# Kernel optimization log

Hardware: AMD Instinct MI355X
Metric: run time of the kernel (lower is better)

Reference implementation:

```python
import jax, jax.numpy as jnp
import numpy as np

N, E, D, L, R, G, C = 50000, 800000, 64, 3, 2, 128, 10


def setup_inputs() -> dict:
    key = jax.random.key(0)
    ks = jax.random.split(key, 16)
    s = 0.05
    x = jax.random.normal(ks[0], (N, D), dtype=jnp.float32)
    edge_index = jax.random.randint(ks[1], (2, E), 0, N, dtype=jnp.int64)
    edge_type = jax.random.randint(ks[2], (E,), 0, R, dtype=jnp.int64)
    batch = jnp.sort(jax.random.randint(ks[3], (N,), 0, G, dtype=jnp.int64))
    # per-layer self-loop Linear, per-(layer,relation) GIN eps + 2-layer MLP
    self_W = jax.random.normal(ks[4], (L, D, D), dtype=jnp.float32) * s
    self_b = jax.random.normal(ks[5], (L, D), dtype=jnp.float32) * s
    eps = jnp.zeros((L, R), dtype=jnp.float32)  # eps=0, train_eps=True
    mlp_W1 = jax.random.normal(ks[6], (L, R, D, D), dtype=jnp.float32) * s
    mlp_b1 = jax.random.normal(ks[7], (L, R, D), dtype=jnp.float32) * s
    mlp_W2 = jax.random.normal(ks[8], (L, R, D, D), dtype=jnp.float32) * s
    mlp_b2 = jax.random.normal(ks[9], (L, R, D), dtype=jnp.float32) * s
    lin1_W = jax.random.normal(ks[10], (D, D), dtype=jnp.float32) * s
    lin1_b = jax.random.normal(ks[11], (D,), dtype=jnp.float32) * s
    lin2_W = jax.random.normal(ks[12], (D, C), dtype=jnp.float32) * s
    lin2_b = jax.random.normal(ks[13], (C,), dtype=jnp.float32) * s
    return {"x": x, "edge_index": edge_index, "edge_type": edge_type, "batch": batch,
            "self_W": self_W, "self_b": self_b, "eps": eps,
            "mlp_W1": mlp_W1, "mlp_b1": mlp_b1, "mlp_W2": mlp_W2, "mlp_b2": mlp_b2,
            "lin1_W": lin1_W, "lin1_b": lin1_b, "lin2_W": lin2_W, "lin2_b": lin2_b}


def reference(x, edge_index, edge_type, batch, self_W, self_b, eps,
              mlp_W1, mlp_b1, mlp_W2, mlp_b2, lin1_W, lin1_b, lin2_W, lin2_b):
    src, dst = edge_index[0], edge_index[1]
    h = x
    for l in range(L):
        x_new = h @ self_W[l] + self_b[l]
        x_src = h[src]  # [E, D] gather of source features, done once per layer
        for r in range(R):
            # per-relation edge masking + scatter-add aggregation
            msg = jnp.where((edge_type == r)[:, None], x_src, jnp.zeros((), h.dtype))
            agg = jax.ops.segment_sum(msg, dst, num_segments=N)  # [N, D]
            z = (1.0 + eps[l, r]) * h + agg  # GIN combine
            z = jax.nn.relu(z @ mlp_W1[l, r] + mlp_b1[l, r])
            x_new = x_new + (z @ mlp_W2[l, r] + mlp_b2[l, r])
        h = x_new
    # global mean pooling over graphs
    sums = jax.ops.segment_sum(h, batch, num_segments=G)  # [G, D]
    counts = jax.ops.segment_sum(jnp.ones((N,), h.dtype), batch, num_segments=G)
    pooled = sums / jnp.maximum(counts, 1.0)[:, None]
    out = jax.nn.relu(pooled @ lin1_W + lin1_b)
    # dropout omitted (eval mode)
    out = out @ lin2_W + lin2_b
    return out
```

## Files before the change

### kernel.cpp

```cpp
#include <hip/hip_runtime.h>

#define Nn 50000
#define Dd 64
#define Ee 800000
#define Ll 3
#define Rr 2
#define Gg 128
#define Cc 10
#define NR (Nn * Rr)
#define NB ((NR + 1023) / 1024)
#define NT (Nn / 16)

typedef __attribute__((ext_vector_type(8))) short short8;
typedef __attribute__((ext_vector_type(4))) float f32x4;

__device__ __forceinline__ unsigned short bf16_rne(float x) {
  unsigned u = __float_as_uint(x);
  unsigned r = u + 0x7fffu + ((u >> 16) & 1u);
  return (unsigned short)(r >> 16);
}
__device__ __forceinline__ float bf16_tof(unsigned short b) {
  return __uint_as_float(((unsigned)b) << 16);
}

__global__ __launch_bounds__(256) void k_hist(
    const int* __restrict__ dst, const int* __restrict__ et,
    int* __restrict__ counts)
{
  int e = blockIdx.x * 256 + threadIdx.x;
  if (e >= Ee) return;
  atomicAdd(&counts[et[e] * Nn + dst[e]], 1);
}

__global__ __launch_bounds__(1024) void k_scan1(
    const int* __restrict__ counts, int* __restrict__ offs,
    int* __restrict__ btot)
{
  __shared__ int s[1024];
  int i = blockIdx.x * 1024 + threadIdx.x;
  int v = (i < NR) ? counts[i] : 0;
  s[threadIdx.x] = v;
  __syncthreads();
#pragma unroll
  for (int d = 1; d < 1024; d <<= 1) {
    int t = (threadIdx.x >= d) ? s[threadIdx.x - d] : 0;
    __syncthreads();
    s[threadIdx.x] += t;
    __syncthreads();
  }
  if (i < NR) offs[i + 1] = s[threadIdx.x];
  if (threadIdx.x == 1023) btot[blockIdx.x] = s[1023];
}

__global__ __launch_bounds__(128) void k_scan2(
    const int* __restrict__ btot, int* __restrict__ bscan)
{
  __shared__ int s[128];
  int v = (threadIdx.x < NB) ? btot[threadIdx.x] : 0;
  s[threadIdx.x] = v;
  __syncthreads();
#pragma unroll
  for (int d = 1; d < 128; d <<= 1) {
    int t = (threadIdx.x >= d) ? s[threadIdx.x - d] : 0;
    __syncthreads();
    s[threadIdx.x] += t;
    __syncthreads();
  }
  if (threadIdx.x < NB) bscan[threadIdx.x] = s[threadIdx.x] - v;
}

__global__ __launch_bounds__(1024) void k_scan3(
    const int* __restrict__ counts, const int* __restrict__ bscan,
    int* __restrict__ offs, int* __restrict__ cursor)
{
  int i = blockIdx.x * 1024 + threadIdx.x;
  if (i >= NR) return;
  int o = offs[i + 1] + bscan[blockIdx.x];
  offs[i + 1] = o;
  cursor[i] = o - counts[i];
  if (i == 0) offs[0] = 0;
}

__global__ __launch_bounds__(256) void k_fill(
    const int* __restrict__ src, const int* __restrict__ dst,
    const int* __restrict__ et, int* __restrict__ cursor,
    int* __restrict__ elist)
{
  int e = blockIdx.x * 256 + threadIdx.x;
  if (e >= Ee) return;
  int pos = atomicAdd(&cursor[et[e] * Nn + dst[e]], 1);
  elist[pos] = src[e];
}

__global__ __launch_bounds__(256) void k_prep(
    const float* __restrict__ selfW, const float* __restrict__ W1,
    const float* __restrict__ W2, unsigned short* __restrict__ wtHi,
    unsigned short* __restrict__ wtLo)
{
  int i = blockIdx.x * 256 + threadIdx.x;
  if (i >= Ll * 5 * 4096) return;
  int l = i / (5 * 4096);
  int rem = i - l * 5 * 4096;
  int m = rem >> 12;
  int e = rem & 4095;
  int k = e >> 6, c = e & 63;
  const float* p;
  if (m == 0)      p = selfW + (size_t)l * 4096;
  else if (m == 1) p = W1 + ((size_t)l * 2 + 0) * 4096;
  else if (m == 2) p = W2 + ((size_t)l * 2 + 0) * 4096;
  else if (m == 3) p = W1 + ((size_t)l * 2 + 1) * 4096;
  else             p = W2 + ((size_t)l * 2 + 1) * 4096;
  float w = p[e];
  unsigned short hi = bf16_rne(w);
  unsigned short lo = bf16_rne(w - bf16_tof(hi));
  size_t o = ((size_t)(l * 5 + m) * 64 + c) * 64 + k;
  wtHi[o] = hi;
  wtLo[o] = lo;
}

#define WOFF(m, c, ks) ((size_t)(m)*4096 + (size_t)(c)*64 + (ks)*32 + koff)

__global__ __launch_bounds__(128, 6) void k_update(
    const float* __restrict__ h, const int* __restrict__ offs,
    const int* __restrict__ elist,
    const unsigned short* __restrict__ wtHi, const unsigned short* __restrict__ wtLo,
    const float* __restrict__ selfb, const float* __restrict__ eps,
    const float* __restrict__ b1, const float* __restrict__ b2,
    float* __restrict__ hn, int l)
{
  __shared__ __align__(16) unsigned short tbh[2][16 * 72];
  __shared__ __align__(16) unsigned short tbl[2][16 * 72];
  __shared__ float xfer[16 * 65];
  const int wave = threadIdx.x >> 6;
  const int lane = threadIdx.x & 63;
  const int task = blockIdx.x;
  const int r = wave;
  const int idx15 = lane & 15;
  const int kg = lane >> 4;
  const int koff = kg * 8;
  const int nodeA = task * 16 + idx15;

  float f[2][8];
  {
    const float* hp = &h[(size_t)nodeA * 64 + koff];
    const float4 a0 = *(const float4*)(hp);
    const float4 a1 = *(const float4*)(hp + 4);
    const float4 b0 = *(const float4*)(hp + 32);
    const float4 b1v = *(const float4*)(hp + 36);
    f[0][0] = a0.x; f[0][1] = a0.y; f[0][2] = a0.z; f[0][3] = a0.w;
    f[0][4] = a1.x; f[0][5] = a1.y; f[0][6] = a1.z; f[0][7] = a1.w;
    f[1][0] = b0.x; f[1][1] = b0.y; f[1][2] = b0.z; f[1][3] = b0.w;
    f[1][4] = b1v.x; f[1][5] = b1v.y; f[1][6] = b1v.z; f[1][7] = b1v.w;
  }

  const unsigned short* whi = wtHi + (size_t)l * 5 * 4096;
  const unsigned short* wlo = wtLo + (size_t)l * 5 * 4096;
  const int m1 = 1 + 2 * r, m2 = 2 + 2 * r;
  const float er = 1.0f + eps[l * Rr + r];

  float za[2][8];
#pragma unroll
  for (int ks = 0; ks < 2; ++ks)
#pragma unroll
    for (int j = 0; j < 8; ++j) za[ks][j] = 0.0f;
  {
    int aidx = r * Nn + nodeA;
    int jb = offs[aidx], je = offs[aidx + 1];
    int j = jb;
    for (; j + 3 < je; j += 4) {
      int s0 = elist[j], s1 = elist[j + 1], s2 = elist[j + 2], s3 = elist[j + 3];
      const float* p0 = &h[(size_t)s0 * 64 + koff];
      const float* p1 = &h[(size_t)s1 * 64 + koff];
      const float* p2 = &h[(size_t)s2 * 64 + koff];
      const float* p3 = &h[(size_t)s3 * 64 + koff];
      const float4 a0 = *(const float4*)(p0),     a1 = *(const float4*)(p1);
      const float4 a2 = *(const float4*)(p2),     a3 = *(const float4*)(p3);
      const float4 b0 = *(const float4*)(p0 + 4), b1q = *(const float4*)(p1 + 4);
      const float4 b2q = *(const float4*)(p2 + 4), b3 = *(const float4*)(p3 + 4);
      const float4 c0 = *(const float4*)(p0 + 32), c1 = *(const float4*)(p1 + 32);
      const float4 c2 = *(const float4*)(p2 + 32), c3 = *(const float4*)(p3 + 32);
      const float4 d0 = *(const float4*)(p0 + 36), d1 = *(const float4*)(p1 + 36);
      const float4 d2 = *(const float4*)(p2 + 36), d3 = *(const float4*)(p3 + 36);
      za[0][0] += (a0.x + a1.x) + (a2.x + a3.x);
      za[0][1] += (a0.y + a1.y) + (a2.y + a3.y);
      za[0][2] += (a0.z + a1.z) + (a2.z + a3.z);
      za[0][3] += (a0.w + a1.w) + (a2.w + a3.w);
      za[0][4] += (b0.x + b1q.x) + (b2q.x + b3.x);
      za[0][5] += (b0.y + b1q.y) + (b2q.y + b3.y);
      za[0][6] += (b0.z + b1q.z) + (b2q.z + b3.z);
      za[0][7] += (b0.w + b1q.w) + (b2q.w + b3.w);
      za[1][0] += (c0.x + c1.x) + (c2.x + c3.x);
      za[1][1] += (c0.y + c1.y) + (c2.y + c3.y);
      za[1][2] += (c0.z + c1.z) + (c2.z + c3.z);
      za[1][3] += (c0.w + c1.w) + (c2.w + c3.w);
      za[1][4] += (d0.x + d1.x) + (d2.x + d3.x);
      za[1][5] += (d0.y + d1.y) + (d2.y + d3.y);
      za[1][6] += (d0.z + d1.z) + (d2.z + d3.z);
      za[1][7] += (d0.w + d1.w) + (d2.w + d3.w);
    }
    for (; j < je; ++j) {
      int sn = elist[j];
      const float* hp = &h[(size_t)sn * 64 + koff];
      const float4 a0 = *(const float4*)(hp);
      const float4 a1 = *(const float4*)(hp + 4);
      const float4 b0 = *(const float4*)(hp + 32);
      const float4 b1v = *(const float4*)(hp + 36);
      za[0][0] += a0.x; za[0][1] += a0.y; za[0][2] += a0.z; za[0][3] += a0.w;
      za[0][4] += a1.x; za[0][5] += a1.y; za[0][6] += a1.z; za[0][7] += a1.w;
      za[1][0] += b0.x; za[1][1] += b0.y; za[1][2] += b0.z; za[1][3] += b0.w;
      za[1][4] += b1v.x; za[1][5] += b1v.y; za[1][6] += b1v.z; za[1][7] += b1v.w;
    }
  }

  short8 zhi[2], zlo[2];
#pragma unroll
  for (int ks = 0; ks < 2; ++ks)
#pragma unroll
    for (int j = 0; j < 8; ++j) {
      float zf = er * f[ks][j] + za[ks][j];
      unsigned short hb = bf16_rne(zf);
      zhi[ks][j] = (short)hb;
      zlo[ks][j] = (short)bf16_rne(zf - bf16_tof(hb));
    }

  f32x4 tacc[4];
#pragma unroll
  for (int cb = 0; cb < 4; ++cb) {
    float bi = b1[((size_t)l * 2 + r) * 64 + cb * 16 + idx15];
    tacc[cb] = (f32x4){bi, bi, bi, bi};
  }
#pragma unroll
  for (int cb = 0; cb < 4; ++cb) {
    int c = cb * 16 + idx15;
#pragma unroll
    for (int ks = 0; ks < 2; ++ks) {
      const short8 bh = *(const short8*)&whi[WOFF(m1, c, ks)];
      const short8 bl = *(const short8*)&wlo[WOFF(m1, c, ks)];
      tacc[cb] = __builtin_amdgcn_mfma_f32_16x16x32_bf16(zhi[ks], bh, tacc[cb], 0, 0, 0);
      tacc[cb] = __builtin_amdgcn_mfma_f32_16x16x32_bf16(zhi[ks], bl, tacc[cb], 0, 0, 0);
      tacc[cb] = __builtin_amdgcn_mfma_f32_16x16x32_bf16(zlo[ks], bh, tacc[cb], 0, 0, 0);
    }
  }
#pragma unroll
  for (int cb = 0; cb < 4; ++cb)
#pragma unroll
    for (int q = 0; q < 4; ++q) {
      float tv = fmaxf(tacc[cb][q], 0.0f);
      unsigned short hb = bf16_rne(tv);
      tbh[wave][(kg * 4 + q) * 72 + cb * 16 + idx15] = hb;
      tbl[wave][(kg * 4 + q) * 72 + cb * 16 + idx15] = bf16_rne(tv - bf16_tof(hb));
    }
  asm volatile("s_waitcnt lgkmcnt(0)" ::: "memory");
  __builtin_amdgcn_sched_barrier(0);
  short8 thi[2], tlo[2];
#pragma unroll
  for (int ks = 0; ks < 2; ++ks) {
    thi[ks] = *(const short8*)&tbh[wave][idx15 * 72 + ks * 32 + koff];
    tlo[ks] = *(const short8*)&tbl[wave][idx15 * 72 + ks * 32 + koff];
  }

  f32x4 facc[4];
#pragma unroll
  for (int cb = 0; cb < 4; ++cb) {
    int c = cb * 16 + idx15;
    float bi = b2[((size_t)l * 2 + r) * 64 + c];
    if (wave == 1) bi += selfb[l * 64 + c];
    facc[cb] = (f32x4){bi, bi, bi, bi};
  }
#pragma unroll
  for (int cb = 0; cb < 4; ++cb) {
    int c = cb * 16 + idx15;
#pragma unroll
    for (int ks = 0; ks < 2; ++ks) {
      const short8 bh = *(const short8*)&whi[WOFF(m2, c, ks)];
      const short8 bl = *(const short8*)&wlo[WOFF(m2, c, ks)];
      facc[cb] = __builtin_amdgcn_mfma_f32_16x16x32_bf16(thi[ks], bh, facc[cb], 0, 0, 0);
      facc[cb] = __builtin_amdgcn_mfma_f32_16x16x32_bf16(thi[ks], bl, facc[cb], 0, 0, 0);
      facc[cb] = __builtin_amdgcn_mfma_f32_16x16x32_bf16(tlo[ks], bh, facc[cb], 0, 0, 0);
    }
  }
  if (wave == 1) {
    short8 ahi[2], alo[2];
#pragma unroll
    for (int ks = 0; ks < 2; ++ks)
#pragma unroll
      for (int j = 0; j < 8; ++j) {
        unsigned short hb = bf16_rne(f[ks][j]);
        ahi[ks][j] = (short)hb;
        alo[ks][j] = (short)bf16_rne(f[ks][j] - bf16_tof(hb));
      }
#pragma unroll
    for (int cb = 0; cb < 4; ++cb) {
      int c = cb * 16 + idx15;
#pragma unroll
      for (int ks = 0; ks < 2; ++ks) {
        const short8 bh = *(const short8*)&whi[WOFF(0, c, ks)];
        const short8 bl = *(const short8*)&wlo[WOFF(0, c, ks)];
        facc[cb] = __builtin_amdgcn_mfma_f32_16x16x32_bf16(ahi[ks], bh, facc[cb], 0, 0, 0);
        facc[cb] = __builtin_amdgcn_mfma_f32_16x16x32_bf16(ahi[ks], bl, facc[cb], 0, 0, 0);
        facc[cb] = __builtin_amdgcn_mfma_f32_16x16x32_bf16(alo[ks], bh, facc[cb], 0, 0, 0);
      }
    }
#pragma unroll
    for (int cb = 0; cb < 4; ++cb)
#pragma unroll
      for (int q = 0; q < 4; ++q)
        xfer[(kg * 4 + q) * 65 + cb * 16 + idx15] = facc[cb][q];
  }
  __syncthreads();
  if (wave == 0) {
#pragma unroll
    for (int cb = 0; cb < 4; ++cb)
#pragma unroll
      for (int q = 0; q < 4; ++q) {
        int row = kg * 4 + q, col = cb * 16 + idx15;
        hn[((size_t)task * 16 + row) * 64 + col] =
            facc[cb][q] + xfer[row * 65 + col];
      }
  }
}

__global__ __launch_bounds__(256) void k_pool(
    const float* __restrict__ h, const int* __restrict__ batch,
    float* __restrict__ sums, float* __restrict__ cnts)
{
  int w = blockIdx.x * 4 + (threadIdx.x >> 6);
  int lane = threadIdx.x & 63;
  int start = w * 64;
  if (start >= Nn) return;
  int cnt = min(64, Nn - start);
  int bg = batch[min(start + lane, Nn - 1)];
  int cur = __shfl(bg, 0, 64);
  float acc = 0.0f;
  int run = 0;
  for (int i = 0; i < cnt; ++i) {
    int g = __shfl(bg, i, 64);
    float v = h[(size_t)(start + i) * 64 + lane];
    if (g != cur) {
      atomicAdd(&sums[(size_t)cur * 64 + lane], acc);
      if (lane == 0) atomicAdd(&cnts[cur], (float)run);
      acc = 0.0f; run = 0; cur = g;
    }
    acc += v; run++;
  }
  atomicAdd(&sums[(size_t)cur * 64 + lane], acc);
  if (lane == 0) atomicAdd(&cnts[cur], (float)run);
}

__global__ __launch_bounds__(256) void k_head(
    const float* __restrict__ sums, const float* __restrict__ cnts,
    const float* __restrict__ l1W, const float* __restrict__ l1b,
    const float* __restrict__ l2W, const float* __restrict__ l2b,
    float* __restrict__ out)
{
  int wave = threadIdx.x >> 6;
  int lane = threadIdx.x & 63;
  int g = blockIdx.x * 4 + wave;
  if (g >= Gg) return;
  float p = sums[(size_t)g * Dd + lane] / fmaxf(cnts[g], 1.0f);
  float t = l1b[lane];
#pragma unroll
  for (int k = 0; k < Dd; ++k)
    t += __shfl(p, k, 64) * l1W[k * Dd + lane];
  t = fmaxf(t, 0.0f);
  float o = (lane < Cc) ? l2b[lane] : 0.0f;
#pragma unroll
  for (int k = 0; k < Dd; ++k) {
    float w = (lane < Cc) ? l2W[k * Cc + lane] : 0.0f;
    o += __shfl(t, k, 64) * w;
  }
  if (lane < Cc) out[(size_t)g * Cc + lane] = o;
}

extern "C" void kernel_launch(void* const* d_in, const int* in_sizes, int n_in,
                              void* d_out, int out_size, void* d_ws, size_t ws_size,
                              hipStream_t stream)
{
  const float* x     = (const float*)d_in[0];
  const int*   ei    = (const int*)d_in[1];
  const int*   et    = (const int*)d_in[2];
  const int*   batch = (const int*)d_in[3];
  const float* selfW = (const float*)d_in[4];
  const float* selfb = (const float*)d_in[5];
  const float* eps   = (const float*)d_in[6];
  const float* W1    = (const float*)d_in[7];
  const float* b1    = (const float*)d_in[8];
  const float* W2    = (const float*)d_in[9];
  const float* b2    = (const float*)d_in[10];
  const float* l1W   = (const float*)d_in[11];
  const float* l1b   = (const float*)d_in[12];
  const float* l2W   = (const float*)d_in[13];
  const float* l2b   = (const float*)d_in[14];
  float* out = (float*)d_out;

  float* buf0 = (float*)d_ws;
  float* buf1 = buf0 + (size_t)Nn * Dd;
  float* sums = buf1 + (size_t)Nn * Dd;
  float* cnts = sums + (size_t)Gg * Dd;
  unsigned short* wtHi = (unsigned short*)(cnts + Gg);
  unsigned short* wtLo = wtHi + (size_t)Ll * 5 * 4096;
  int* counts = (int*)(wtLo + (size_t)Ll * 5 * 4096);
  int* offs   = counts + NR;
  int* cursor = offs + NR + 1;
  int* btot   = cursor + NR;
  int* bscan  = btot + NB;
  int* elist  = bscan + NB;

  const int* src = ei;
  const int* dst = ei + Ee;

  hipMemsetAsync(sums, 0, (size_t)(Gg * Dd + Gg) * sizeof(float), stream);
  hipMemsetAsync(counts, 0, (size_t)NR * sizeof(int), stream);
  k_prep<<<(Ll * 5 * 4096 + 255) / 256, 256, 0, stream>>>(selfW, W1, W2, wtHi, wtLo);

  k_hist<<<(Ee + 255) / 256, 256, 0, stream>>>(dst, et, counts);
  k_scan1<<<NB, 1024, 0, stream>>>(counts, offs, btot);
  k_scan2<<<1, 128, 0, stream>>>(btot, bscan);
  k_scan3<<<NB, 1024, 0, stream>>>(counts, bscan, offs, cursor);
  k_fill<<<(Ee + 255) / 256, 256, 0, stream>>>(src, dst, et, cursor, elist);

  const float* h = x;
  float* hn = buf0;
  for (int l = 0; l < Ll; ++l) {
    k_update<<<NT, 128, 0, stream>>>(h, offs, elist, wtHi, wtLo,
                                     selfb, eps, b1, b2, hn, l);
    h = hn;
    hn = (hn == buf0) ? buf1 : buf0;
  }
  k_pool<<<(Nn / 64 + 4) / 4, 256, 0, stream>>>(h, batch, sums, cnts);
  k_head<<<32, 256, 0, stream>>>(sums, cnts, l1W, l1b, l2W, l2b, out);
}
```

Baseline: 338.1 us.

## Gather neighbor features from a bf16 shadow copy to halve gather bandwidth

Keeps a bf16 copy of node features alongside the fp32 buffer. Each layer writes both, and a new conversion kernel fills it for the input. The edge aggregation gathers bf16 rows, which halves the bytes read per neighbor in the bandwidth-bound gather. In exchange it adds an extra store per layer and a conversion pass, lowers the occupancy hint from 6 to 5, and loses precision in the aggregated sums, since neighbors are summed at bf16 resolution.

```diff
diff --git a/kernel.cpp b/kernel.cpp
--- a/kernel.cpp
+++ b/kernel.cpp
@@ -22,6 +22,16 @@
 __device__ __forceinline__ float bf16_tof(unsigned short b) {
   return __uint_as_float(((unsigned)b) << 16);
 }
+__device__ __forceinline__ void acc8(float* z, uint4 u) {
+  z[0] += __uint_as_float(u.x << 16);
+  z[1] += __uint_as_float(u.x & 0xffff0000u);
+  z[2] += __uint_as_float(u.y << 16);
+  z[3] += __uint_as_float(u.y & 0xffff0000u);
+  z[4] += __uint_as_float(u.z << 16);
+  z[5] += __uint_as_float(u.z & 0xffff0000u);
+  z[6] += __uint_as_float(u.w << 16);
+  z[7] += __uint_as_float(u.w & 0xffff0000u);
+}
 
 __global__ __launch_bounds__(256) void k_hist(
     const int* __restrict__ dst, const int* __restrict__ et,
@@ -90,6 +100,18 @@
   if (e >= Ee) return;
   int pos = atomicAdd(&cursor[et[e] * Nn + dst[e]], 1);
   elist[pos] = src[e];
+}
+
+__global__ __launch_bounds__(256) void k_cvt(
+    const float* __restrict__ x, unsigned short* __restrict__ hb)
+{
+  int i = blockIdx.x * 256 + threadIdx.x;
+  if (i >= (Nn * Dd) / 4) return;
+  const float4 v = *(const float4*)&x[(size_t)i * 4];
+  ushort4 o;
+  o.x = bf16_rne(v.x); o.y = bf16_rne(v.y);
+  o.z = bf16_rne(v.z); o.w = bf16_rne(v.w);
+  *(ushort4*)&hb[(size_t)i * 4] = o;
 }
 
 __global__ __launch_bounds__(256) void k_prep(
@@ -120,13 +142,13 @@
 
 #define WOFF(m, c, ks) ((size_t)(m)*4096 + (size_t)(c)*64 + (ks)*32 + koff)
 
-__global__ __launch_bounds__(128, 6) void k_update(
-    const float* __restrict__ h, const int* __restrict__ offs,
-    const int* __restrict__ elist,
+__global__ __launch_bounds__(128, 5) void k_update(
+    const float* __restrict__ h, const unsigned short* __restrict__ hb,
+    const int* __restrict__ offs, const int* __restrict__ elist,
     const unsigned short* __restrict__ wtHi, const unsigned short* __restrict__ wtLo,
     const float* __restrict__ selfb, const float* __restrict__ eps,
     const float* __restrict__ b1, const float* __restrict__ b2,
-    float* __restrict__ hn, int l)
+    float* __restrict__ hn, unsigned short* __restrict__ hnb, int l)
 {
   __shared__ __align__(16) unsigned short tbh[2][16 * 72];
   __shared__ __align__(16) unsigned short tbl[2][16 * 72];
@@ -169,46 +191,26 @@
     int j = jb;
     for (; j + 3 < je; j += 4) {
       int s0 = elist[j], s1 = elist[j + 1], s2 = elist[j + 2], s3 = elist[j + 3];
-      const float* p0 = &h[(size_t)s0 * 64 + koff];
-      const float* p1 = &h[(size_t)s1 * 64 + koff];
-      const float* p2 = &h[(size_t)s2 * 64 + koff];
-      const float* p3 = &h[(size_t)s3 * 64 + koff];
-      const float4 a0 = *(const float4*)(p0),     a1 = *(const float4*)(p1);
-      const float4 a2 = *(const float4*)(p2),     a3 = *(const float4*)(p3);
-      const float4 b0 = *(const float4*)(p0 + 4), b1q = *(const float4*)(p1 + 4);
-      const float4 b2q = *(const float4*)(p2 + 4), b3 = *(const float4*)(p3 + 4);
-      const float4 c0 = *(const float4*)(p0 + 32), c1 = *(const float4*)(p1 + 32);
-      const float4 c2 = *(const float4*)(p2 + 32), c3 = *(const float4*)(p3 + 32);
-      const float4 d0 = *(const float4*)(p0 + 36), d1 = *(const float4*)(p1 + 36);
-      const float4 d2 = *(const float4*)(p2 + 36), d3 = *(const float4*)(p3 + 36);
-      za[0][0] += (a0.x + a1.x) + (a2.x + a3.x);
-      za[0][1] += (a0.y + a1.y) + (a2.y + a3.y);
-      za[0][2] += (a0.z + a1.z) + (a2.z + a3.z);
-      za[0][3] += (a0.w + a1.w) + (a2.w + a3.w);
-      za[0][4] += (b0.x + b1q.x) + (b2q.x + b3.x);
-      za[0][5] += (b0.y + b1q.y) + (b2q.y + b3.y);
-      za[0][6] += (b0.z + b1q.z) + (b2q.z + b3.z);
-      za[0][7] += (b0.w + b1q.w) + (b2q.w + b3.w);
-      za[1][0] += (c0.x + c1.x) + (c2.x + c3.x);
-      za[1][1] += (c0.y + c1.y) + (c2.y + c3.y);
-      za[1][2] += (c0.z + c1.z) + (c2.z + c3.z);
-      za[1][3] += (c0.w + c1.w) + (c2.w + c3.w);
-      za[1][4] += (d0.x + d1.x) + (d2.x + d3.x);
-      za[1][5] += (d0.y + d1.y) + (d2.y + d3.y);
-      za[1][6] += (d0.z + d1.z) + (d2.z + d3.z);
-      za[1][7] += (d0.w + d1.w) + (d2.w + d3.w);
+      const unsigned short* q0 = &hb[(size_t)s0 * 64 + koff];
+      const unsigned short* q1 = &hb[(size_t)s1 * 64 + koff];
+      const unsigned short* q2 = &hb[(size_t)s2 * 64 + koff];
+      const unsigned short* q3 = &hb[(size_t)s3 * 64 + koff];
+      const uint4 a0 = *(const uint4*)(q0);
+      const uint4 a1 = *(const uint4*)(q1);
+      const uint4 a2 = *(const uint4*)(q2);
+      const uint4 a3 = *(const uint4*)(q3);
+      const uint4 b0 = *(const uint4*)(q0 + 32);
+      const uint4 b1q = *(const uint4*)(q1 + 32);
+      const uint4 b2q = *(const uint4*)(q2 + 32);
+      const uint4 b3 = *(const uint4*)(q3 + 32);
+      acc8(za[0], a0); acc8(za[0], a1); acc8(za[0], a2); acc8(za[0], a3);
+      acc8(za[1], b0); acc8(za[1], b1q); acc8(za[1], b2q); acc8(za[1], b3);
     }
     for (; j < je; ++j) {
-      int sn = elist[j];
-      const float* hp = &h[(size_t)sn * 64 + koff];
-      const float4 a0 = *(const float4*)(hp);
-      const float4 a1 = *(const float4*)(hp + 4);
-      const float4 b0 = *(const float4*)(hp + 32);
-      const float4 b1v = *(const float4*)(hp + 36);
-      za[0][0] += a0.x; za[0][1] += a0.y; za[0][2] += a0.z; za[0][3] += a0.w;
-      za[0][4] += a1.x; za[0][5] += a1.y; za[0][6] += a1.z; za[0][7] += a1.w;
-      za[1][0] += b0.x; za[1][1] += b0.y; za[1][2] += b0.z; za[1][3] += b0.w;
-      za[1][4] += b1v.x; za[1][5] += b1v.y; za[1][6] += b1v.z; za[1][7] += b1v.w;
+      const unsigned short* q = &hb[(size_t)elist[j] * 64 + koff];
+      const uint4 a = *(const uint4*)(q);
+      const uint4 b = *(const uint4*)(q + 32);
+      acc8(za[0], a); acc8(za[1], b);
     }
   }
 
@@ -218,9 +220,9 @@
 #pragma unroll
     for (int j = 0; j < 8; ++j) {
       float zf = er * f[ks][j] + za[ks][j];
-      unsigned short hb = bf16_rne(zf);
-      zhi[ks][j] = (short)hb;
-      zlo[ks][j] = (short)bf16_rne(zf - bf16_tof(hb));
+      unsigned short hb2 = bf16_rne(zf);
+      zhi[ks][j] = (short)hb2;
+      zlo[ks][j] = (short)bf16_rne(zf - bf16_tof(hb2));
     }
 
   f32x4 tacc[4];
@@ -246,9 +248,9 @@
 #pragma unroll
     for (int q = 0; q < 4; ++q) {
       float tv = fmaxf(tacc[cb][q], 0.0f);
-      unsigned short hb = bf16_rne(tv);
-      tbh[wave][(kg * 4 + q) * 72 + cb * 16 + idx15] = hb;
-      tbl[wave][(kg * 4 + q) * 72 + cb * 16 + idx15] = bf16_rne(tv - bf16_tof(hb));
+      unsigned short hb2 = bf16_rne(tv);
+      tbh[wave][(kg * 4 + q) * 72 + cb * 16 + idx15] = hb2;
+      tbl[wave][(kg * 4 + q) * 72 + cb * 16 + idx15] = bf16_rne(tv - bf16_tof(hb2));
     }
   asm volatile("s_waitcnt lgkmcnt(0)" ::: "memory");
   __builtin_amdgcn_sched_barrier(0);
@@ -285,9 +287,9 @@
     for (int ks = 0; ks < 2; ++ks)
 #pragma unroll
       for (int j = 0; j < 8; ++j) {
-        unsigned short hb = bf16_rne(f[ks][j]);
-        ahi[ks][j] = (short)hb;
-        alo[ks][j] = (short)bf16_rne(f[ks][j] - bf16_tof(hb));
+        unsigned short hb2 = bf16_rne(f[ks][j]);
+        ahi[ks][j] = (short)hb2;
+        alo[ks][j] = (short)bf16_rne(f[ks][j] - bf16_tof(hb2));
       }
 #pragma unroll
     for (int cb = 0; cb < 4; ++cb) {
@@ -314,8 +316,10 @@
 #pragma unroll
       for (int q = 0; q < 4; ++q) {
         int row = kg * 4 + q, col = cb * 16 + idx15;
-        hn[((size_t)task * 16 + row) * 64 + col] =
-            facc[cb][q] + xfer[row * 65 + col];
+        float v = facc[cb][q] + xfer[row * 65 + col];
+        size_t o = ((size_t)task * 16 + row) * 64 + col;
+        hn[o] = v;
+        hnb[o] = bf16_rne(v);
       }
   }
 }
@@ -395,7 +399,9 @@
 
   float* buf0 = (float*)d_ws;
   float* buf1 = buf0 + (size_t)Nn * Dd;
-  float* sums = buf1 + (size_t)Nn * Dd;
+  unsigned short* hb0 = (unsigned short*)(buf1 + (size_t)Nn * Dd);
+  unsigned short* hb1 = hb0 + (size_t)Nn * Dd;
+  float* sums = (float*)(hb1 + (size_t)Nn * Dd);
   float* cnts = sums + (size_t)Gg * Dd;
   unsigned short* wtHi = (unsigned short*)(cnts + Gg);
   unsigned short* wtLo = wtHi + (size_t)Ll * 5 * 4096;
@@ -412,6 +418,7 @@
   hipMemsetAsync(sums, 0, (size_t)(Gg * Dd + Gg) * sizeof(float), stream);
   hipMemsetAsync(counts, 0, (size_t)NR * sizeof(int), stream);
   k_prep<<<(Ll * 5 * 4096 + 255) / 256, 256, 0, stream>>>(selfW, W1, W2, wtHi, wtLo);
+  k_cvt<<<(Nn * Dd / 4 + 255) / 256, 256, 0, stream>>>(x, hb0);
 
   k_hist<<<(Ee + 255) / 256, 256, 0, stream>>>(dst, et, counts);
   k_scan1<<<NB, 1024, 0, stream>>>(counts, offs, btot);
@@ -420,12 +427,16 @@
   k_fill<<<(Ee + 255) / 256, 256, 0, stream>>>(src, dst, et, cursor, elist);
 
   const float* h = x;
+  const unsigned short* hbc = hb0;
   float* hn = buf0;
+  unsigned short* hnb = hb1;
   for (int l = 0; l < Ll; ++l) {
-    k_update<<<NT, 128, 0, stream>>>(h, offs, elist, wtHi, wtLo,
-                                     selfb, eps, b1, b2, hn, l);
+    k_update<<<NT, 128, 0, stream>>>(h, hbc, offs, elist, wtHi, wtLo,
+                                     selfb, eps, b1, b2, hn, hnb, l);
     h = hn;
+    hbc = hnb;
     hn = (hn == buf0) ? buf1 : buf0;
+    hnb = (hnb == hb0) ? hb1 : hb0;
   }
   k_pool<<<(Nn / 64 + 4) / 4, 256, 0, stream>>>(h, batch, sums, cnts);
   k_head<<<32, 256, 0, stream>>>(sums, cnts, l1W, l1b, l2W, l2b, out);
```

After: 296.8 us. 12.2% less time.
